# Kernel optimization log

Measured on AMD Instinct MI355X. Metric: run time of the kernel, lower is better.

Reference implementation:

```python
import jax, jax.numpy as jnp
import numpy as np

MEAN = jnp.array([0.4914, 0.4822, 0.4465], dtype=jnp.float32)
STD = jnp.array([0.2023, 0.1994, 0.201], dtype=jnp.float32)


def conv2d(x, w, b, stride, pad):
    out = jax.lax.conv_general_dilated(
        x, w, (stride, stride), [(pad, pad), (pad, pad)],
        dimension_numbers=('NCHW', 'OIHW', 'NCHW'))
    return out + b[None, :, None, None]


def topk_select(out_list, scores):
    # SubNet zeros the lowest int(0.75*N) |scores|; SelectNet gathers the
    # surviving channels in original channel order.
    N = scores.shape[1]
    keep = N - int(0.75 * N)
    _, idx = jax.lax.top_k(scores, keep)
    idx = jnp.sort(idx, axis=1)  # boolean-mask gather preserves order
    if out_list.ndim == 4:
        return jnp.take_along_axis(out_list, idx[:, :, None, None], axis=1)
    return jnp.take_along_axis(out_list, idx, axis=1)


def moe_conv(x, We, be, Wr, br, stride, pad):
    B = x.shape[0]
    out = conv2d(x, We.reshape((-1,) + We.shape[2:]), be.reshape(-1), stride, pad)
    scores = jnp.abs(x.reshape(B, -1) @ Wr + br)
    return topk_select(out, scores)


def moe_linear(x, We, be, Wr, br):
    out = (jnp.einsum('bi,eoi->beo', x, We) + be[None]).reshape(x.shape[0], -1)
    scores = jnp.abs(x @ Wr + br)
    return topk_select(out, scores)


def setup_inputs():
    key = jax.random.key(0)
    ks = iter(jax.random.split(key, 32))

    def w(shape, fan_in):
        return jax.random.normal(next(ks), shape, jnp.float32) / np.sqrt(fan_in)

    B = 1024
    inp = {'x': jax.random.uniform(next(ks), (B, 3, 32, 32), jnp.float32)}
    inp['W0'] = w((32, 3, 3, 3), 27);        inp['b0'] = jnp.zeros((32,), jnp.float32)
    inp['W2'] = w((32, 32, 4, 4), 512);      inp['b2'] = jnp.zeros((32,), jnp.float32)
    inp['W4'] = w((64, 32, 3, 3), 288);      inp['b4'] = jnp.zeros((64,), jnp.float32)
    inp['W6e'] = w((4, 64, 64, 4, 4), 1024); inp['b6e'] = jnp.zeros((4, 64), jnp.float32)
    inp['Wr6'] = w((64 * 16 * 16, 256), 16384); inp['br6'] = jnp.zeros((256,), jnp.float32)
    inp['W9e'] = w((4, 512, 4096), 4096);    inp['b9e'] = jnp.zeros((4, 512), jnp.float32)
    inp['Wr9'] = w((4096, 2048), 4096);      inp['br9'] = jnp.zeros((2048,), jnp.float32)
    inp['W11e'] = w((4, 512, 512), 512);     inp['b11e'] = jnp.zeros((4, 512), jnp.float32)
    inp['Wr11'] = w((512, 2048), 512);       inp['br11'] = jnp.zeros((2048,), jnp.float32)
    inp['W13e'] = w((4, 10, 512), 512);      inp['b13e'] = jnp.zeros((4, 10), jnp.float32)
    inp['Wr13'] = w((512, 40), 512);         inp['br13'] = jnp.zeros((40,), jnp.float32)
    return inp


def reference(x, W0, b0, W2, b2, W4, b4,
              W6e, b6e, Wr6, br6,
              W9e, b9e, Wr9, br9,
              W11e, b11e, Wr11, br11,
              W13e, b13e, Wr13, br13):
    x = (x - MEAN[None, :, None, None]) / STD[None, :, None, None]
    out = jax.nn.relu(conv2d(x, W0, b0, 1, 1))      # [B,32,32,32]
    out = jax.nn.relu(conv2d(out, W2, b2, 2, 1))    # [B,32,16,16]
    out = jax.nn.relu(conv2d(out, W4, b4, 1, 1))    # [B,64,16,16]
    out = jax.nn.relu(moe_conv(out, W6e, b6e, Wr6, br6, 2, 1))  # [B,64,8,8]
    out = out.reshape(out.shape[0], -1)             # [B,4096]
    out = jax.nn.relu(moe_linear(out, W9e, b9e, Wr9, br9))      # [B,512]
    out = jax.nn.relu(moe_linear(out, W11e, b11e, Wr11, br11))  # [B,512]
    return moe_linear(out, W13e, b13e, Wr13, br13)  # [B,10]
```

## Files before the change

### kernel.cpp

```cpp
#include <hip/hip_runtime.h>
#include <stdint.h>

#define DEV __device__ __forceinline__

typedef __attribute__((ext_vector_type(8))) short bf16x8;
typedef __attribute__((ext_vector_type(8))) unsigned short u16x8;
typedef __attribute__((ext_vector_type(4))) float f32x4;

DEV unsigned short rne1(float f, float& rem) {
  uint32_t u = __float_as_uint(f);
  uint32_t t = (u + 0x7fffu + ((u >> 16) & 1u)) & 0xffff0000u;
  rem = f - __uint_as_float(t);
  return (unsigned short)(t >> 16);
}
DEV void split3(float f, unsigned short& a0, unsigned short& a1, unsigned short& a2) {
  float r1, r2;
  a0 = rne1(f, r1);
  a1 = rne1(r1, r2);
  uint32_t u = __float_as_uint(r2);
  a2 = (unsigned short)((u + 0x7fffu + ((u >> 16) & 1u)) >> 16);
}
DEV void split3_4(float4 v, ushort4& h0, ushort4& h1, ushort4& h2) {
  split3(v.x, h0.x, h1.x, h2.x);
  split3(v.y, h0.y, h1.y, h2.y);
  split3(v.z, h0.z, h1.z, h2.z);
  split3(v.w, h0.w, h1.w, h2.w);
}

__global__ __launch_bounds__(256) void k_conv0(
    const float* __restrict__ x, const float* __restrict__ W,
    const float* __restrict__ b, float* __restrict__ y0, int base)
{
  __shared__ float sIn[3][34][34];
  const int t = threadIdx.x;
  const long img = base + blockIdx.x;
  const float mean[3] = {0.4914f, 0.4822f, 0.4465f};
  const float stdv[3] = {0.2023f, 0.1994f, 0.201f};
  for (int i = t; i < 3 * 34 * 34; i += 256) {
    int c = i / 1156, r = i % 1156, yy = r / 34 - 1, xx = r % 34 - 1;
    float v = 0.f;
    if ((unsigned)yy < 32u && (unsigned)xx < 32u)
      v = (x[((img * 3 + c) * 32 + yy) * 32 + xx] - mean[c]) / stdv[c];
    (&sIn[0][0][0])[i] = v;
  }
  __syncthreads();
  for (int p = t; p < 1024; p += 256) {
    const int py = p >> 5, px = p & 31;
    float in[27];
#pragma unroll
    for (int c = 0; c < 3; c++)
#pragma unroll
      for (int ky = 0; ky < 3; ky++)
#pragma unroll
        for (int kx = 0; kx < 3; kx++)
          in[c * 9 + ky * 3 + kx] = sIn[c][py + ky][px + kx];
#pragma unroll 4
    for (int oc = 0; oc < 32; oc++) {
      float acc = b[oc];
      const float* wp = W + oc * 27;
#pragma unroll
      for (int k = 0; k < 27; k++) acc += in[k] * wp[k];
      y0[(((long)blockIdx.x * 32 + oc) * 32 + py) * 32 + px] = fmaxf(acc, 0.f);
    }
  }
}

__global__ __launch_bounds__(256, 2) void k_conv2m(
    const float* __restrict__ y0, const float* __restrict__ W2,
    const float* __restrict__ bb, float* __restrict__ y2)
{
  __shared__ __align__(16) unsigned short sB[3][256][40];
  const int t = threadIdx.x;
  const int lane = t & 63, wid = t >> 6;
  const int fr = lane & 15, kg = lane >> 4;
  const long img = blockIdx.x;
  const int py = t >> 4, px = t & 15;
  const float* yimg = y0 + img * (32 * 1024);

  f32x4 acc[2][4];
#pragma unroll
  for (int i = 0; i < 2; i++)
#pragma unroll
    for (int j = 0; j < 4; j++) acc[i][j] = (f32x4)0.f;

#pragma unroll 1
  for (int ks = 0; ks < 16; ks++) {
    __syncthreads();
#pragma unroll
    for (int icL = 0; icL < 2; icL++) {
      const int ic = ks * 2 + icL;
#pragma unroll
      for (int ky = 0; ky < 4; ky++) {
        const int iy = 2 * py + ky - 1;
        float v[4];
#pragma unroll
        for (int kx = 0; kx < 4; kx++) {
          const int ix = 2 * px + kx - 1;
          v[kx] = ((unsigned)iy < 32u && (unsigned)ix < 32u)
                    ? yimg[(ic * 32 + iy) * 32 + ix] : 0.f;
        }
        ushort4 h0, h1, h2;
        split3_4(make_float4(v[0], v[1], v[2], v[3]), h0, h1, h2);
        const int kloc = icL * 16 + ky * 4;
        *(ushort4*)&sB[0][t][kloc] = h0;
        *(ushort4*)&sB[1][t][kloc] = h1;
        *(ushort4*)&sB[2][t][kloc] = h2;
      }
    }
    __syncthreads();

    bf16x8 bfv[3][4];
#pragma unroll
    for (int s = 0; s < 3; s++)
#pragma unroll
      for (int nf = 0; nf < 4; nf++)
        bfv[s][nf] = *(const bf16x8*)&sB[s][wid * 64 + nf * 16 + fr][kg * 8];

#pragma unroll
    for (int mf = 0; mf < 2; mf++) {
      const float* wr = W2 + (long)(mf * 16 + fr) * 512 + ks * 32 + kg * 8;
      float4 w0 = *(const float4*)wr;
      float4 w1 = *(const float4*)(wr + 4);
      ushort4 p0, p1, p2, q0, q1, q2;
      split3_4(w0, p0, p1, p2);
      split3_4(w1, q0, q1, q2);
      bf16x8 a0, a1, a2;
      a0[0]=(short)p0.x; a0[1]=(short)p0.y; a0[2]=(short)p0.z; a0[3]=(short)p0.w;
      a0[4]=(short)q0.x; a0[5]=(short)q0.y; a0[6]=(short)q0.z; a0[7]=(short)q0.w;
      a1[0]=(short)p1.x; a1[1]=(short)p1.y; a1[2]=(short)p1.z; a1[3]=(short)p1.w;
      a1[4]=(short)q1.x; a1[5]=(short)q1.y; a1[6]=(short)q1.z; a1[7]=(short)q1.w;
      a2[0]=(short)p2.x; a2[1]=(short)p2.y; a2[2]=(short)p2.z; a2[3]=(short)p2.w;
      a2[4]=(short)q2.x; a2[5]=(short)q2.y; a2[6]=(short)q2.z; a2[7]=(short)q2.w;
#pragma unroll
      for (int nf = 0; nf < 4; nf++) {
        f32x4 a = acc[mf][nf];
        a = __builtin_amdgcn_mfma_f32_16x16x32_bf16(a1, bfv[1][nf], a, 0, 0, 0);
        a = __builtin_amdgcn_mfma_f32_16x16x32_bf16(a0, bfv[2][nf], a, 0, 0, 0);
        a = __builtin_amdgcn_mfma_f32_16x16x32_bf16(a2, bfv[0][nf], a, 0, 0, 0);
        a = __builtin_amdgcn_mfma_f32_16x16x32_bf16(a1, bfv[0][nf], a, 0, 0, 0);
        a = __builtin_amdgcn_mfma_f32_16x16x32_bf16(a0, bfv[1][nf], a, 0, 0, 0);
        a = __builtin_amdgcn_mfma_f32_16x16x32_bf16(a0, bfv[0][nf], a, 0, 0, 0);
        acc[mf][nf] = a;
      }
    }
  }
#pragma unroll
  for (int mf = 0; mf < 2; mf++)
#pragma unroll
    for (int nf = 0; nf < 4; nf++) {
      const int pix = wid * 64 + nf * 16 + fr;
#pragma unroll
      for (int reg = 0; reg < 4; reg++) {
        const int oc = mf * 16 + kg * 4 + reg;
        y2[(img * 32 + oc) * 256 + pix] = fmaxf(acc[mf][nf][reg] + bb[oc], 0.f);
      }
    }
}

__global__ __launch_bounds__(256) void k_splitW4(
    const float* __restrict__ W, unsigned short* __restrict__ Wsp)
{
  const int i = blockIdx.x * 256 + threadIdx.x;
  if (i >= 64 * 288) return;
  const int o = i / 288, r = i % 288, ic = r / 9, tap = r % 9;
  unsigned short a0, a1, a2;
  split3(W[i], a0, a1, a2);
  const int base = (tap * 64 + o) * 32 + ic;
  Wsp[base] = a0;
  Wsp[18432 + base] = a1;
  Wsp[36864 + base] = a2;
}

__global__ __launch_bounds__(256, 2) void k_conv4m(
    const float* __restrict__ y2, const unsigned short* __restrict__ Wsp,
    const float* __restrict__ bb, float* __restrict__ y4)
{
  __shared__ __align__(16) unsigned short sX[3][324][40];
  const int t = threadIdx.x;
  const int lane = t & 63, wid = t >> 6;
  const int fr = lane & 15, kg = lane >> 4;
  const long img = blockIdx.x;
  const float* yimg = y2 + img * (32 * 256);

  for (int i = t; i < 324 * 32; i += 256) {
    const int ic = i / 324, pos = i % 324;
    const int iy = pos / 18, ix = pos % 18;
    float v = 0.f;
    if ((unsigned)(iy - 1) < 16u && (unsigned)(ix - 1) < 16u)
      v = yimg[(ic * 16 + iy - 1) * 16 + ix - 1];
    unsigned short a0, a1, a2;
    split3(v, a0, a1, a2);
    sX[0][pos][ic] = a0;
    sX[1][pos][ic] = a1;
    sX[2][pos][ic] = a2;
  }
  __syncthreads();

  f32x4 acc[4][4];
#pragma unroll
  for (int i = 0; i < 4; i++)
#pragma unroll
    for (int j = 0; j < 4; j++) acc[i][j] = (f32x4)0.f;

  const int pyb = wid * 4;
#pragma unroll 1
  for (int tap = 0; tap < 9; tap++) {
    const int ky = tap / 3, kx = tap % 3;
    bf16x8 bfv[3][4];
#pragma unroll
    for (int s = 0; s < 3; s++)
#pragma unroll
      for (int nf = 0; nf < 4; nf++)
        bfv[s][nf] = *(const bf16x8*)&sX[s][(pyb + nf + ky) * 18 + fr + kx][kg * 8];
#pragma unroll
    for (int mf = 0; mf < 4; mf++) {
      const int wb = (tap * 64 + mf * 16 + fr) * 32 + kg * 8;
      bf16x8 a0 = *(const bf16x8*)&Wsp[wb];
      bf16x8 a1 = *(const bf16x8*)&Wsp[18432 + wb];
      bf16x8 a2 = *(const bf16x8*)&Wsp[36864 + wb];
#pragma unroll
      for (int nf = 0; nf < 4; nf++) {
        f32x4 a = acc[mf][nf];
        a = __builtin_amdgcn_mfma_f32_16x16x32_bf16(a1, bfv[1][nf], a, 0, 0, 0);
        a = __builtin_amdgcn_mfma_f32_16x16x32_bf16(a0, bfv[2][nf], a, 0, 0, 0);
        a = __builtin_amdgcn_mfma_f32_16x16x32_bf16(a2, bfv[0][nf], a, 0, 0, 0);
        a = __builtin_amdgcn_mfma_f32_16x16x32_bf16(a1, bfv[0][nf], a, 0, 0, 0);
        a = __builtin_amdgcn_mfma_f32_16x16x32_bf16(a0, bfv[1][nf], a, 0, 0, 0);
        a = __builtin_amdgcn_mfma_f32_16x16x32_bf16(a0, bfv[0][nf], a, 0, 0, 0);
        acc[mf][nf] = a;
      }
    }
  }
#pragma unroll
  for (int mf = 0; mf < 4; mf++)
#pragma unroll
    for (int nf = 0; nf < 4; nf++) {
      const int p2 = wid * 64 + nf * 16 + fr;
#pragma unroll
      for (int reg = 0; reg < 4; reg++) {
        const int oc = mf * 16 + kg * 4 + reg;
        y4[(img * 64 + oc) * 256 + p2] = fmaxf(acc[mf][nf][reg] + bb[oc], 0.f);
      }
    }
}

__global__ __launch_bounds__(256) void k_splitW(
    const float* __restrict__ W, unsigned short* __restrict__ Wsp)
{
  const int i = (blockIdx.x * 256 + threadIdx.x) * 4;
  float4 v = *(const float4*)&W[i];
  ushort4 h0, h1, h2; split3_4(v, h0, h1, h2);
  *(ushort4*)&Wsp[i]          = h0;
  *(ushort4*)&Wsp[262144 + i] = h1;
  *(ushort4*)&Wsp[524288 + i] = h2;
}

__global__ __launch_bounds__(256) void k_conv6m(
    const float* __restrict__ y4, const unsigned short* __restrict__ Wsp,
    const float* __restrict__ bb, float* __restrict__ c6)
{
  __shared__ __align__(16) unsigned short sB[3][64][56];
  const int t = threadIdx.x;
  const int lane = t & 63, wid = t >> 6;
  const int fr = lane & 15, kg = lane >> 4;
  const long img = blockIdx.x;
  const int pix = t >> 2, q = t & 3;
  const int spy = pix >> 3, spx = pix & 7;
  const int icL = q >> 1, kyB = (q & 1) * 2;
  const float* yimg = y4 + img * (64 * 256);

  f32x4 acc[4][4];
#pragma unroll
  for (int i = 0; i < 4; i++)
#pragma unroll
    for (int j = 0; j < 4; j++) acc[i][j] = (f32x4)0.f;

#pragma unroll 1
  for (int ks = 0; ks < 32; ks++) {
    const int ic = ks * 2 + icL;
    float v[8];
#pragma unroll
    for (int j = 0; j < 8; j++) {
      const int ky = kyB + (j >> 2), kx = j & 3;
      const int iy = 2 * spy + ky - 1, ix = 2 * spx + kx - 1;
      v[j] = ((unsigned)iy < 16u && (unsigned)ix < 16u)
               ? yimg[(ic * 16 + iy) * 16 + ix] : 0.f;
    }
    u16x8 h0, h1, h2;
#pragma unroll
    for (int j = 0; j < 8; j++) {
      unsigned short a0, a1, a2;
      split3(v[j], a0, a1, a2);
      h0[j] = a0; h1[j] = a1; h2[j] = a2;
    }
    __syncthreads();
    *(u16x8*)&sB[0][pix][q * 8] = h0;
    *(u16x8*)&sB[1][pix][q * 8] = h1;
    *(u16x8*)&sB[2][pix][q * 8] = h2;
    __syncthreads();

    bf16x8 bfv[3][4];
#pragma unroll
    for (int s = 0; s < 3; s++)
#pragma unroll
      for (int nf = 0; nf < 4; nf++)
        bfv[s][nf] = *(const bf16x8*)&sB[s][nf * 16 + fr][kg * 8];

    const int kbase = ks * 32 + kg * 8;
#pragma unroll
    for (int mf = 0; mf < 4; mf++) {
      const int oc = wid * 64 + mf * 16 + fr;
      bf16x8 a0 = *(const bf16x8*)&Wsp[(long)oc * 1024 + kbase];
      bf16x8 a1 = *(const bf16x8*)&Wsp[(long)(256 + oc) * 1024 + kbase];
      bf16x8 a2 = *(const bf16x8*)&Wsp[(long)(512 + oc) * 1024 + kbase];
#pragma unroll
      for (int nf = 0; nf < 4; nf++) {
        f32x4 a = acc[mf][nf];
        a = __builtin_amdgcn_mfma_f32_16x16x32_bf16(a1, bfv[1][nf], a, 0, 0, 0);
        a = __builtin_amdgcn_mfma_f32_16x16x32_bf16(a0, bfv[2][nf], a, 0, 0, 0);
        a = __builtin_amdgcn_mfma_f32_16x16x32_bf16(a2, bfv[0][nf], a, 0, 0, 0);
        a = __builtin_amdgcn_mfma_f32_16x16x32_bf16(a1, bfv[0][nf], a, 0, 0, 0);
        a = __builtin_amdgcn_mfma_f32_16x16x32_bf16(a0, bfv[1][nf], a, 0, 0, 0);
        a = __builtin_amdgcn_mfma_f32_16x16x32_bf16(a0, bfv[0][nf], a, 0, 0, 0);
        acc[mf][nf] = a;
      }
    }
  }
#pragma unroll
  for (int mf = 0; mf < 4; mf++)
#pragma unroll
    for (int nf = 0; nf < 4; nf++) {
      const int ocb = wid * 64 + mf * 16 + kg * 4;
      const int p2 = nf * 16 + fr;
#pragma unroll
      for (int reg = 0; reg < 4; reg++) {
        const int oc = ocb + reg;
        c6[(img * 256 + oc) * 64 + p2] = acc[mf][nf][reg] + bb[oc];
      }
    }
}

template<int B_NK, int DO_ABS, int SPLITK>
__global__ __launch_bounds__(256, 4) void k_sgemm(
    const float* __restrict__ A, const float* __restrict__ Bm,
    const float* __restrict__ bias, float* __restrict__ C,
    int M, int N, int K)
{
  __shared__ float As[16][68];
  __shared__ float Bs[16][68];
  const int t = threadIdx.x;
  const int tx = t & 15, ty = t >> 4;
  const int n0 = blockIdx.x * 64, m0 = blockIdx.y * 64;
  const int Kc = K / SPLITK;
  const int k0 = blockIdx.z * Kc;
  float acc[4][4] = {{0.f}};
  for (int kt = 0; kt < Kc; kt += 16) {
    __syncthreads();
    {
      const int kc = t & 15, r0 = t >> 4;
#pragma unroll
      for (int i = 0; i < 4; i++)
        As[kc][r0 + 16 * i] = A[(long)(m0 + r0 + 16 * i) * K + k0 + kt + kc];
      if (B_NK) {
#pragma unroll
        for (int i = 0; i < 4; i++)
          Bs[kc][r0 + 16 * i] = Bm[(long)(n0 + r0 + 16 * i) * K + k0 + kt + kc];
      } else {
        const int nc = t & 63, kr0 = t >> 6;
#pragma unroll
        for (int i = 0; i < 4; i++)
          Bs[kr0 + 4 * i][nc] = Bm[(long)(k0 + kt + kr0 + 4 * i) * N + n0 + nc];
      }
    }
    __syncthreads();
    float part[4][4] = {{0.f}};
#pragma unroll
    for (int k = 0; k < 16; k++) {
      float4 av = *(const float4*)&As[k][ty * 4];
      float4 bv = *(const float4*)&Bs[k][tx * 4];
      const float a[4] = {av.x, av.y, av.z, av.w};
      const float bb[4] = {bv.x, bv.y, bv.z, bv.w};
#pragma unroll
      for (int i = 0; i < 4; i++)
#pragma unroll
        for (int j = 0; j < 4; j++)
          part[i][j] += a[i] * bb[j];
    }
#pragma unroll
    for (int i = 0; i < 4; i++)
#pragma unroll
      for (int j = 0; j < 4; j++)
        acc[i][j] += part[i][j];
  }
#pragma unroll
  for (int i = 0; i < 4; i++) {
    const long m = m0 + ty * 4 + i;
    float vv[4];
#pragma unroll
    for (int j = 0; j < 4; j++) {
      float u = acc[i][j];
      if (SPLITK == 1) {
        u += bias[n0 + tx * 4 + j];
        if (DO_ABS) u = fabsf(u);
      }
      vv[j] = u;
    }
    float4 v; v.x = vv[0]; v.y = vv[1]; v.z = vv[2]; v.w = vv[3];
    float* dst = (SPLITK == 1) ? &C[m * N + n0 + tx * 4]
                               : &C[((long)blockIdx.z * M + m) * N + n0 + tx * 4];
    *(float4*)dst = v;
  }
}

template<int B_NK, int DO_ABS, int SPLITK>
__global__ __launch_bounds__(256, 2) void k_mgemm(
    const float* __restrict__ A, const float* __restrict__ Bm,
    const float* __restrict__ bias, float* __restrict__ C,
    int M, int N, int K)
{
  __shared__ __align__(16) unsigned short sA[3][64][40];
  __shared__ __align__(16) unsigned short sB[3][128][40];
  const int t = threadIdx.x;
  const int n0 = blockIdx.x * 128, m0 = blockIdx.y * 64;
  const int Kc = K / SPLITK;
  const int k0 = blockIdx.z * Kc;
  const int lane = t & 63, wid = t >> 6;
  const int wm = wid >> 1, wn = wid & 1;
  const int fr = lane & 15, kg = lane >> 4;

  f32x4 acc[2][4];
#pragma unroll
  for (int i = 0; i < 2; i++)
#pragma unroll
    for (int j = 0; j < 4; j++) acc[i][j] = (f32x4)0.f;

  for (int kt = 0; kt < Kc; kt += 32) {
    __syncthreads();
    {
      const int kq = t & 7, r = t >> 3;
#pragma unroll
      for (int i = 0; i < 2; i++) {
        float4 v = *(const float4*)&A[(long)(m0 + r + 32 * i) * K + k0 + kt + kq * 4];
        ushort4 h0, h1, h2; split3_4(v, h0, h1, h2);
        *(ushort4*)&sA[0][r + 32 * i][kq * 4] = h0;
        *(ushort4*)&sA[1][r + 32 * i][kq * 4] = h1;
        *(ushort4*)&sA[2][r + 32 * i][kq * 4] = h2;
      }
    }
    if (B_NK) {
      const int kq = t & 7, r = t >> 3;
#pragma unroll
      for (int i = 0; i < 4; i++) {
        float4 v = *(const float4*)&Bm[(long)(n0 + r + 32 * i) * K + k0 + kt + kq * 4];
        ushort4 h0, h1, h2; split3_4(v, h0, h1, h2);
        *(ushort4*)&sB[0][r + 32 * i][kq * 4] = h0;
        *(ushort4*)&sB[1][r + 32 * i][kq * 4] = h1;
        *(ushort4*)&sB[2][r + 32 * i][kq * 4] = h2;
      }
    } else {
      const int nq = t & 31, kr = t >> 5;
#pragma unroll
      for (int i = 0; i < 4; i++) {
        const int k = kr + 8 * i;
        float4 v = *(const float4*)&Bm[(long)(k0 + kt + k) * N + n0 + nq * 4];
        ushort4 h0, h1, h2; split3_4(v, h0, h1, h2);
        sB[0][nq * 4 + 0][k] = h0.x; sB[1][nq * 4 + 0][k] = h1.x; sB[2][nq * 4 + 0][k] = h2.x;
        sB[0][nq * 4 + 1][k] = h0.y; sB[1][nq * 4 + 1][k] = h1.y; sB[2][nq * 4 + 1][k] = h2.y;
        sB[0][nq * 4 + 2][k] = h0.z; sB[1][nq * 4 + 2][k] = h1.z; sB[2][nq * 4 + 2][k] = h2.z;
        sB[0][nq * 4 + 3][k] = h0.w; sB[1][nq * 4 + 3][k] = h1.w; sB[2][nq * 4 + 3][k] = h2.w;
      }
    }
    __syncthreads();

    bf16x8 af[3][2], bfv[3][4];
#pragma unroll
    for (int s = 0; s < 3; s++)
#pragma unroll
      for (int mf = 0; mf < 2; mf++)
        af[s][mf] = *(const bf16x8*)&sA[s][wm * 32 + mf * 16 + fr][kg * 8];
#pragma unroll
    for (int s = 0; s < 3; s++)
#pragma unroll
      for (int nf = 0; nf < 4; nf++)
        bfv[s][nf] = *(const bf16x8*)&sB[s][wn * 64 + nf * 16 + fr][kg * 8];

#pragma unroll
    for (int mf = 0; mf < 2; mf++)
#pragma unroll
      for (int nf = 0; nf < 4; nf++) {
        f32x4 a = acc[mf][nf];
        a = __builtin_amdgcn_mfma_f32_16x16x32_bf16(af[1][mf], bfv[1][nf], a, 0, 0, 0);
        a = __builtin_amdgcn_mfma_f32_16x16x32_bf16(af[0][mf], bfv[2][nf], a, 0, 0, 0);
        a = __builtin_amdgcn_mfma_f32_16x16x32_bf16(af[2][mf], bfv[0][nf], a, 0, 0, 0);
        a = __builtin_amdgcn_mfma_f32_16x16x32_bf16(af[1][mf], bfv[0][nf], a, 0, 0, 0);
        a = __builtin_amdgcn_mfma_f32_16x16x32_bf16(af[0][mf], bfv[1][nf], a, 0, 0, 0);
        a = __builtin_amdgcn_mfma_f32_16x16x32_bf16(af[0][mf], bfv[0][nf], a, 0, 0, 0);
        acc[mf][nf] = a;
      }
  }

  float* dst = (SPLITK == 1) ? C : C + (long)blockIdx.z * M * N;
#pragma unroll
  for (int mf = 0; mf < 2; mf++)
#pragma unroll
    for (int nf = 0; nf < 4; nf++) {
      const int n = n0 + wn * 64 + nf * 16 + fr;
      const int mb = m0 + wm * 32 + mf * 16 + kg * 4;
#pragma unroll
      for (int reg = 0; reg < 4; reg++) {
        float u = acc[mf][nf][reg];
        if (SPLITK == 1) {
          u += bias[n];
          if (DO_ABS) u = fabsf(u);
        }
        dst[(long)(mb + reg) * N + n] = u;
      }
    }
}

__global__ __launch_bounds__(256) void k_reduce6(
    const float* __restrict__ part, const float* __restrict__ br,
    float* __restrict__ s6, int rows)
{
  const int i = blockIdx.x * 256 + threadIdx.x;
  const int tot = rows * 256;
  if (i < tot) {
    float s = br[i & 255];
#pragma unroll
    for (int z = 0; z < 16; z++) s += part[z * tot + i];
    s6[i] = fabsf(s);
  }
}

__global__ __launch_bounds__(256) void k_reduce9(
    const float* __restrict__ part, const float* __restrict__ br,
    float* __restrict__ s9)
{
  const int i = blockIdx.x * 256 + threadIdx.x;
  const int tot = 1024 * 2048;
  s9[i] = fabsf(part[i] + part[tot + i] + br[i & 2047]);
}

DEV int blk_reduce(int v, volatile int* sW4) {
#pragma unroll
  for (int d = 32; d > 0; d >>= 1) v += __shfl_down(v, d);
  const int lane = threadIdx.x & 63, wid = threadIdx.x >> 6;
  if (lane == 0) sW4[wid] = v;
  __syncthreads();
  int tot = sW4[0] + sW4[1] + sW4[2] + sW4[3];
  __syncthreads();
  return tot;
}

DEV int blk_exscan(int v, volatile int* sW4) {
  const int lane = threadIdx.x & 63, wid = threadIdx.x >> 6;
  int inc = v;
#pragma unroll
  for (int d = 1; d < 64; d <<= 1) {
    int u = __shfl_up(inc, d);
    if (lane >= d) inc += u;
  }
  if (lane == 63) sW4[wid] = inc;
  __syncthreads();
  int off = 0;
#pragma unroll
  for (int w = 0; w < 3; w++)
    if (w < wid) off += sW4[w];
  __syncthreads();
  return off + inc - v;
}

template<int N, int KEEP, int SPATIAL>
__global__ __launch_bounds__(256) void k_topk(
    const float* __restrict__ scores, const float* __restrict__ full,
    float* __restrict__ out)
{
  constexpr int E = N / 256;
  __shared__ int sW4[4];
  __shared__ int sSel[KEEP];
  const int t = threadIdx.x;
  const long row = blockIdx.x;
  uint32_t kk[E];
#pragma unroll
  for (int e = 0; e < E; e++) kk[e] = __float_as_uint(scores[row * N + t * E + e]);
  uint32_t prefix = 0u;
  for (int bit = 31; bit >= 0; bit--) {
    uint32_t cand = prefix | (1u << bit);
    int c = 0;
#pragma unroll
    for (int e = 0; e < E; e++) c += (kk[e] >= cand) ? 1 : 0;
    if (blk_reduce(c, sW4) >= KEEP) prefix = cand;
  }
  int myG = 0, myE = 0;
#pragma unroll
  for (int e = 0; e < E; e++) { myG += kk[e] > prefix; myE += kk[e] == prefix; }
  const int G = blk_reduce(myG, sW4);
  const int needEq = KEEP - G;
  const int prefE = blk_exscan(myE, sW4);
  const int keepcnt = myG + max(0, min(myE, needEq - prefE));
  int pos = blk_exscan(keepcnt, sW4);
  int eqSeen = prefE;
#pragma unroll
  for (int e = 0; e < E; e++) {
    const bool kp = (kk[e] > prefix) || ((kk[e] == prefix) && (eqSeen < needEq));
    if (kk[e] == prefix) eqSeen++;
    if (kp) sSel[pos++] = t * E + e;
  }
  __syncthreads();
  if (SPATIAL) {
    for (int i = t; i < KEEP * 64; i += 256)
      out[row * (KEEP * 64) + i] = fmaxf(full[(row * N + sSel[i >> 6]) * 64 + (i & 63)], 0.f);
  } else {
    for (int i = t; i < KEEP; i += 256)
      out[row * KEEP + i] = fmaxf(full[row * N + sSel[i]], 0.f);
  }
}

__global__ __launch_bounds__(256) void k_final(
    const float* __restrict__ y11, const float* __restrict__ W13,
    const float* __restrict__ b13, const float* __restrict__ Wr13,
    const float* __restrict__ br13, float* __restrict__ outp)
{
  __shared__ float sX[512];
  __shared__ float sL[64];
  __shared__ float sS[64];
  const int t = threadIdx.x;
  const long row = blockIdx.x;
  for (int i = t; i < 512; i += 256) sX[i] = y11[row * 512 + i];
  __syncthreads();
  if (t < 40) {
    float acc = b13[t];
    const float4* w4 = (const float4*)(W13 + t * 512);
    for (int k = 0; k < 128; k++) {
      float4 w = w4[k];
      acc += sX[4 * k] * w.x + sX[4 * k + 1] * w.y + sX[4 * k + 2] * w.z + sX[4 * k + 3] * w.w;
    }
    sL[t] = acc;
  } else if (t >= 64 && t < 104) {
    const int n = t - 64;
    float acc = br13[n];
    for (int k = 0; k < 512; k++) acc += sX[k] * Wr13[k * 40 + n];
    sS[n] = fabsf(acc);
  }
  __syncthreads();
  if (t < 64) {
    const uint32_t key = (t < 40) ? __float_as_uint(sS[t]) : 0u;
    uint32_t prefix = 0u;
#pragma unroll
    for (int bit = 31; bit >= 0; bit--) {
      uint32_t cand = prefix | (1u << bit);
      unsigned long long m = __ballot(t < 40 && key >= cand);
      if (__popcll(m) >= 10) prefix = cand;
    }
    const int G = __popcll(__ballot(t < 40 && key > prefix));
    const int needEq = 10 - G;
    const unsigned long long me = __ballot(t < 40 && key == prefix);
    const unsigned long long lt = (t == 0) ? 0ull : (~0ull >> (64 - t));
    const int eqr = __popcll(me & lt);
    const bool kp = (t < 40) && ((key > prefix) || (key == prefix && eqr < needEq));
    const int pos = __popcll(__ballot(kp) & lt);
    if (kp) outp[row * 10 + pos] = sL[t];
  }
}

extern "C" void kernel_launch(void* const* d_in, const int* in_sizes, int n_in,
                              void* d_out, int out_size, void* d_ws, size_t ws_size,
                              hipStream_t stream)
{
  const float* x    = (const float*)d_in[0];
  const float* W0   = (const float*)d_in[1];
  const float* b0   = (const float*)d_in[2];
  const float* W2   = (const float*)d_in[3];
  const float* b2   = (const float*)d_in[4];
  const float* W4   = (const float*)d_in[5];
  const float* b4   = (const float*)d_in[6];
  const float* W6   = (const float*)d_in[7];
  const float* b6   = (const float*)d_in[8];
  const float* Wr6  = (const float*)d_in[9];
  const float* br6  = (const float*)d_in[10];
  const float* W9   = (const float*)d_in[11];
  const float* b9   = (const float*)d_in[12];
  const float* Wr9  = (const float*)d_in[13];
  const float* br9  = (const float*)d_in[14];
  const float* W11  = (const float*)d_in[15];
  const float* b11  = (const float*)d_in[16];
  const float* Wr11 = (const float*)d_in[17];
  const float* br11 = (const float*)d_in[18];
  const float* W13  = (const float*)d_in[19];
  const float* b13  = (const float*)d_in[20];
  const float* Wr13 = (const float*)d_in[21];
  const float* br13 = (const float*)d_in[22];
  float* out = (float*)d_out;
  float* ws = (float*)d_ws;

  float* R0  = ws;
  float* R1  = ws + 16777216;
  float* y6  = ws + 16777216 + 4194304;
  float* y0c = R0;
  float* y4c = R0;
  float* c6c = R0 + 8388608;
  unsigned short* Wsp4 = (unsigned short*)(R0 + 10485760);
  float* y2c = R1;
  float* s6  = R1;
  float* p6  = R1 + 262144;
  unsigned short* Wsp = (unsigned short*)(R1 + 2359296);
  float* l9  = R0;
  float* s9  = R0 + 2097152;
  float* y9  = R0 + 4194304;
  float* l11 = R0 + 4718592;
  float* s11 = R0 + 6815744;
  float* y11 = R0 + 8912896;
  float* p9  = R0 + 9437184;

  for (int chunk = 0; chunk < 2; chunk++) {
    const int base = chunk * 512;
    k_conv0<<<512, 256, 0, stream>>>(x, W0, b0, y0c, base);
    k_conv2m<<<512, 256, 0, stream>>>(y0c, W2, b2, y2c);
    k_splitW4<<<72, 256, 0, stream>>>(W4, Wsp4);
    k_conv4m<<<512, 256, 0, stream>>>(y2c, Wsp4, b4, y4c);
    k_splitW<<<256, 256, 0, stream>>>(W6, Wsp);
    k_conv6m<<<512, 256, 0, stream>>>(y4c, Wsp, b6, c6c);
    dim3 g6(256 / 64, 512 / 64, 16);
    k_sgemm<0, 0, 16><<<g6, 256, 0, stream>>>(y4c, Wr6, nullptr, p6, 512, 256, 16384);
    k_reduce6<<<512, 256, 0, stream>>>(p6, br6, s6, 512);
    k_topk<256, 64, 1><<<512, 256, 0, stream>>>(s6, c6c, y6 + (long)base * 4096);
  }

  dim3 g9m(16, 16, 1);
  k_mgemm<1, 0, 1><<<g9m, 256, 0, stream>>>(y6, W9, b9, l9, 1024, 2048, 4096);
  dim3 gs9(2048 / 64, 1024 / 64, 2);
  k_sgemm<0, 0, 2><<<gs9, 256, 0, stream>>>(y6, Wr9, nullptr, p9, 1024, 2048, 4096);
  k_reduce9<<<8192, 256, 0, stream>>>(p9, br9, s9);
  k_topk<2048, 512, 0><<<1024, 256, 0, stream>>>(s9, l9, y9);

  k_mgemm<1, 0, 1><<<g9m, 256, 0, stream>>>(y9, W11, b11, l11, 1024, 2048, 512);
  dim3 gs11(2048 / 64, 1024 / 64, 1);
  k_sgemm<0, 1, 1><<<gs11, 256, 0, stream>>>(y9, Wr11, br11, s11, 1024, 2048, 512);
  k_topk<2048, 512, 0><<<1024, 256, 0, stream>>>(s11, l11, y11);

  k_final<<<1024, 256, 0, stream>>>(y11, W13, b13, Wr13, br13, out);
}
```

Before: 1.397 ms.

## Run conv0 on bf16x3 MFMA and double split-K for router-6 GEMM

Replaces the scalar FP32 first convolution with an im2col-style MFMA kernel. Weights and input patches are split into three bf16 parts and combined with six MFMAs to approximate FP32 accuracy. Each image is now spread over four blocks, one per quarter of the pixels. Separately, the split-K factor of the layer-6 router SGEMM goes from 16 to 32 to raise parallelism, which needs a larger partial buffer and new workspace offsets for p6 and s6. The costs are redundant input staging per block, split3 conversion work, and twice the partial-sum traffic in the reduce.

Measured after the change: 1.355 ms. 3.0% less time.

```diff
diff --git a/kernel.cpp b/kernel.cpp
--- a/kernel.cpp
+++ b/kernel.cpp
@@ -27,13 +27,17 @@
   split3(v.w, h0.w, h1.w, h2.w);
 }
 
-__global__ __launch_bounds__(256) void k_conv0(
+__global__ __launch_bounds__(256, 2) void k_conv0m(
     const float* __restrict__ x, const float* __restrict__ W,
     const float* __restrict__ b, float* __restrict__ y0, int base)
 {
   __shared__ float sIn[3][34][34];
+  __shared__ __align__(16) unsigned short sA[3][32][32];
   const int t = threadIdx.x;
+  const int lane = t & 63, wid = t >> 6;
+  const int fr = lane & 15, kg = lane >> 4;
   const long img = base + blockIdx.x;
+  const int q = blockIdx.y;
   const float mean[3] = {0.4914f, 0.4822f, 0.4465f};
   const float stdv[3] = {0.2023f, 0.1994f, 0.201f};
   for (int i = t; i < 3 * 34 * 34; i += 256) {
@@ -43,26 +47,75 @@
       v = (x[((img * 3 + c) * 32 + yy) * 32 + xx] - mean[c]) / stdv[c];
     (&sIn[0][0][0])[i] = v;
   }
-  __syncthreads();
-  for (int p = t; p < 1024; p += 256) {
-    const int py = p >> 5, px = p & 31;
-    float in[27];
-#pragma unroll
-    for (int c = 0; c < 3; c++)
-#pragma unroll
-      for (int ky = 0; ky < 3; ky++)
-#pragma unroll
-        for (int kx = 0; kx < 3; kx++)
-          in[c * 9 + ky * 3 + kx] = sIn[c][py + ky][px + kx];
-#pragma unroll 4
-    for (int oc = 0; oc < 32; oc++) {
-      float acc = b[oc];
-      const float* wp = W + oc * 27;
-#pragma unroll
-      for (int k = 0; k < 27; k++) acc += in[k] * wp[k];
-      y0[(((long)blockIdx.x * 32 + oc) * 32 + py) * 32 + px] = fmaxf(acc, 0.f);
-    }
-  }
+  for (int i = t; i < 32 * 32; i += 256) {
+    const int oc = i >> 5, k = i & 31;
+    float w = (k < 27) ? W[oc * 27 + k] : 0.f;
+    unsigned short a0, a1, a2;
+    split3(w, a0, a1, a2);
+    sA[0][oc][k] = a0; sA[1][oc][k] = a1; sA[2][oc][k] = a2;
+  }
+  __syncthreads();
+
+  f32x4 acc[2][4];
+#pragma unroll
+  for (int i = 0; i < 2; i++)
+#pragma unroll
+    for (int j = 0; j < 4; j++) acc[i][j] = (f32x4)0.f;
+
+  bf16x8 bfv[3][4];
+#pragma unroll
+  for (int nf = 0; nf < 4; nf++) {
+    const int pixel = q * 256 + wid * 64 + nf * 16 + fr;
+    const int py = pixel >> 5, px = pixel & 31;
+    bf16x8 h0, h1, h2;
+#pragma unroll
+    for (int j = 0; j < 8; j++) {
+      const int k = kg * 8 + j;
+      float v = 0.f;
+      if (k < 27) {
+        const int ic = k / 9, tap = k % 9;
+        v = sIn[ic][py + tap / 3][px + tap % 3];
+      }
+      unsigned short a0, a1, a2;
+      split3(v, a0, a1, a2);
+      h0[j] = (short)a0; h1[j] = (short)a1; h2[j] = (short)a2;
+    }
+    bfv[0][nf] = h0; bfv[1][nf] = h1; bfv[2][nf] = h2;
+  }
+
+  bf16x8 af[3][2];
+#pragma unroll
+  for (int s = 0; s < 3; s++)
+#pragma unroll
+    for (int mf = 0; mf < 2; mf++)
+      af[s][mf] = *(const bf16x8*)&sA[s][mf * 16 + fr][kg * 8];
+
+#pragma unroll
+  for (int mf = 0; mf < 2; mf++)
+#pragma unroll
+    for (int nf = 0; nf < 4; nf++) {
+      f32x4 a = acc[mf][nf];
+      a = __builtin_amdgcn_mfma_f32_16x16x32_bf16(af[1][mf], bfv[1][nf], a, 0, 0, 0);
+      a = __builtin_amdgcn_mfma_f32_16x16x32_bf16(af[0][mf], bfv[2][nf], a, 0, 0, 0);
+      a = __builtin_amdgcn_mfma_f32_16x16x32_bf16(af[2][mf], bfv[0][nf], a, 0, 0, 0);
+      a = __builtin_amdgcn_mfma_f32_16x16x32_bf16(af[1][mf], bfv[0][nf], a, 0, 0, 0);
+      a = __builtin_amdgcn_mfma_f32_16x16x32_bf16(af[0][mf], bfv[1][nf], a, 0, 0, 0);
+      a = __builtin_amdgcn_mfma_f32_16x16x32_bf16(af[0][mf], bfv[0][nf], a, 0, 0, 0);
+      acc[mf][nf] = a;
+    }
+
+#pragma unroll
+  for (int mf = 0; mf < 2; mf++)
+#pragma unroll
+    for (int nf = 0; nf < 4; nf++) {
+      const int pixBase = q * 256 + wid * 64 + nf * 16;
+#pragma unroll
+      for (int reg = 0; reg < 4; reg++) {
+        const int oc = mf * 16 + kg * 4 + reg;
+        y0[((long)blockIdx.x * 32 + oc) * 1024 + pixBase + fr] =
+            fmaxf(acc[mf][nf][reg] + b[oc], 0.f);
+      }
+    }
 }
 
 __global__ __launch_bounds__(256, 2) void k_conv2m(
@@ -527,7 +580,7 @@
   if (i < tot) {
     float s = br[i & 255];
 #pragma unroll
-    for (int z = 0; z < 16; z++) s += part[z * tot + i];
+    for (int z = 0; z < 32; z++) s += part[z * tot + i];
     s6[i] = fabsf(s);
   }
 }
@@ -701,9 +754,9 @@
   float* c6c = R0 + 8388608;
   unsigned short* Wsp4 = (unsigned short*)(R0 + 10485760);
   float* y2c = R1;
-  float* s6  = R1;
-  float* p6  = R1 + 262144;
   unsigned short* Wsp = (unsigned short*)(R1 + 2359296);
+  float* p6  = R1;
+  float* s6  = R0;
   float* l9  = R0;
   float* s9  = R0 + 2097152;
   float* y9  = R0 + 4194304;
@@ -714,14 +767,15 @@
 
   for (int chunk = 0; chunk < 2; chunk++) {
     const int base = chunk * 512;
-    k_conv0<<<512, 256, 0, stream>>>(x, W0, b0, y0c, base);
+    dim3 g0(512, 4);
+    k_conv0m<<<g0, 256, 0, stream>>>(x, W0, b0, y0c, base);
     k_conv2m<<<512, 256, 0, stream>>>(y0c, W2, b2, y2c);
     k_splitW4<<<72, 256, 0, stream>>>(W4, Wsp4);
     k_conv4m<<<512, 256, 0, stream>>>(y2c, Wsp4, b4, y4c);
     k_splitW<<<256, 256, 0, stream>>>(W6, Wsp);
     k_conv6m<<<512, 256, 0, stream>>>(y4c, Wsp, b6, c6c);
-    dim3 g6(256 / 64, 512 / 64, 16);
-    k_sgemm<0, 0, 16><<<g6, 256, 0, stream>>>(y4c, Wr6, nullptr, p6, 512, 256, 16384);
+    dim3 g6(256 / 64, 512 / 64, 32);
+    k_sgemm<0, 0, 32><<<g6, 256, 0, stream>>>(y4c, Wr6, nullptr, p6, 512, 256, 16384);
     k_reduce6<<<512, 256, 0, stream>>>(p6, br6, s6, 512);
     k_topk<256, 64, 1><<<512, 256, 0, stream>>>(s6, c6c, y6 + (long)base * 4096);
   }
```
